# Performance work log

Measured on AMD Instinct MI355X. Metric: run time of the kernel, lower is better.

## Reference

```python
import jax, jax.numpy as jnp
import numpy as np

B, D, H, O, K = 8192, 256, 512, 64, 8


def setup_inputs() -> dict:
    key = jax.random.key(0)
    ks = jax.random.split(key, 4)
    s0 = 1.0 / np.sqrt(D)
    s1 = 1.0 / np.sqrt(H)
    return {
        "x": jax.random.normal(ks[0], (B, D), dtype=jnp.float32),
        "W0": jax.random.normal(ks[1], (K, D, H), dtype=jnp.float32) * s0,
        "b0": jnp.zeros((K, H), dtype=jnp.float32),
        "W1": jax.random.normal(ks[2], (K, H, H), dtype=jnp.float32) * s1,
        "b1": jnp.zeros((K, H), dtype=jnp.float32),
        "Wo": jax.random.normal(ks[3], (K, H, O), dtype=jnp.float32) * s1,
        "bo": jnp.zeros((K, O), dtype=jnp.float32),
    }


def reference(x, W0, b0, W1, b1, Wo, bo):
    # Hard one-hot router (non-differentiable int cast, as in the original)
    idx = jnp.mod(jnp.abs(x[:, 7] * 100.0).astype(jnp.int32), K)  # [B]
    att = jax.nn.one_hot(idx, K, dtype=x.dtype)  # [B, K]
    # Dense compute of ALL subpolicy MLPs (faithful to original wasteful scheme)
    h0 = jnp.tanh(jnp.einsum("bd,kdh->kbh", x, W0) + b0[:, None, :])   # [K,B,H]
    h1 = jnp.tanh(jnp.einsum("kbh,khg->kbg", h0, W1) + b1[:, None, :])  # [K,B,H]
    out = jnp.einsum("kbg,kgo->kbo", h1, Wo) + bo[:, None, :]           # [K,B,O]
    # mask with one-hot attention and sum over experts (tf.add_n of masked outputs)
    overall = jnp.einsum("kbo,bk->bo", out, att)                        # [B,O]
    return overall
```

## Files before the change

kernel.cpp:

```cpp
#include <hip/hip_runtime.h>

#define NB 8192
#define ND 256
#define NH 512
#define NO 64
#define NK 8
#define TB 32

typedef unsigned short u16;
using bf16x8 = __attribute__((ext_vector_type(8))) short;
using u16x8  = __attribute__((ext_vector_type(8))) unsigned short;
using f32x4  = __attribute__((ext_vector_type(4))) float;

__device__ __forceinline__ u16 bf16rne(float f) {
    unsigned u = __float_as_uint(f);
    return (u16)((u + 0x7FFFu + ((u >> 16) & 1u)) >> 16);
}

__device__ __forceinline__ float fast_tanh(float v) {
    float a = fabsf(v);
    float e = __expf(-2.0f * a);
    float t = (1.0f - e) * __builtin_amdgcn_rcpf(1.0f + e);
    return copysignf(t, v);
}


__global__ __launch_bounds__(256) void prep_kernel(
    const float* __restrict__ x,
    const float* __restrict__ W0, const float* __restrict__ W1, const float* __restrict__ Wo,
    int* __restrict__ wsI, u16* __restrict__ W0F, u16* __restrict__ W1F, u16* __restrict__ WoF) {
    const int bid = blockIdx.x, t = threadIdx.x;
    if (bid >= 832) {
        __shared__ int lc[NK], lbase[NK];
        if (t < NK) lc[t] = 0;
        __syncthreads();
        const int b = (bid - 832) * 256 + t;
        const float v = x[(size_t)b * ND + 7];
        const int e = ((int)fabsf(v * 100.0f)) & (NK - 1);
        const int slot = atomicAdd(&lc[e], 1);
        __syncthreads();
        if (t < NK) lbase[t] = atomicAdd(&wsI[t], lc[t]);
        __syncthreads();
        wsI[16 + e * NB + lbase[e] + slot] = b;
        return;
    }
    __shared__ u16 tile[64][76];
    const float* src; u16* dst; int C, NT, r0, c0;
    if (bid < 256) {
        int e = bid >> 5, tt = bid & 31; C = NH; NT = 32;
        src = W0 + (size_t)e * ND * NH; dst = W0F + (size_t)e * ND * NH;
        r0 = (tt >> 3) * 64; c0 = (tt & 7) * 64;
    } else if (bid < 768) {
        int i = bid - 256, e = i >> 6, tt = i & 63; C = NH; NT = 32;
        src = W1 + (size_t)e * NH * NH; dst = W1F + (size_t)e * NH * NH;
        r0 = (tt >> 3) * 64; c0 = (tt & 7) * 64;
    } else {
        int i = bid - 768, e = i >> 3, tt = i & 7; C = NO; NT = 4;
        src = Wo + (size_t)e * NH * NO; dst = WoF + (size_t)e * NH * NO;
        r0 = tt * 64; c0 = 0;
    }
    {
        const int r = t >> 2, cc = (t & 3) * 16;
        const float* p = src + (size_t)(r0 + r) * C + c0 + cc;
#pragma unroll
        for (int j = 0; j < 16; j += 4) {
            float4 v = *(const float4*)(p + j);
            ushort4 h;
            h.x = bf16rne(v.x); h.y = bf16rne(v.y); h.z = bf16rne(v.z); h.w = bf16rne(v.w);
            *(ushort4*)&tile[r][cc + j] = h;
        }
    }
    __syncthreads();
    {
#pragma unroll
        for (int i = 0; i < 2; ++i) {
            const int f = t + i * 256;
            const int lane = f & 63, s = f >> 6;
            const int ktl = s >> 2, ntl = s & 3;
            const int kt = (r0 >> 5) + ktl, nt = (c0 >> 4) + ntl;
            const int kloc = ktl * 32 + (lane >> 4) * 8, nloc = ntl * 16 + (lane & 15);
            u16x8 fr;
#pragma unroll
            for (int q = 0; q < 8; ++q) fr[q] = tile[kloc + q][nloc];
            *(u16x8*)(dst + (size_t)(((kt * NT + nt) << 6) + lane) * 8) = fr;
        }
    }
}

__global__ __launch_bounds__(512, 4) void mlp_kernel(
    const float* __restrict__ x,
    const float* __restrict__ b0, const float* __restrict__ b1, const float* __restrict__ bo,
    const int* __restrict__ wsI,
    const u16* __restrict__ W0F, const u16* __restrict__ W1F, const u16* __restrict__ WoF,
    float* __restrict__ out) {
    const int e = blockIdx.x & (NK - 1);
    const int tile = blockIdx.x >> 3;
    const int cnt = wsI[e];
    if (tile * TB >= cnt) return;

    __shared__ u16 L[32768];
    __shared__ int rows_s[TB];
    const int t = threadIdx.x;
    const int* bucket = wsI + 16 + e * NB;
    if (t < TB) {
        int lr = tile * TB + t;
        rows_s[t] = (lr < cnt) ? bucket[lr] : -1;
    }
    __syncthreads();

#pragma unroll
    for (int s = 0; s < 4; ++s) {
        int i = t + s * 512;
        int row = i >> 6, d4 = i & 63;
        int g = rows_s[row];
        float4 v = (g >= 0) ? *(const float4*)(x + (size_t)g * ND + d4 * 4)
                            : make_float4(0.f, 0.f, 0.f, 0.f);
        ushort4 h;
        h.x = bf16rne(v.x); h.y = bf16rne(v.y); h.z = bf16rne(v.z); h.w = bf16rne(v.w);
        int bb = (row * 512 + d4 * 8) ^ ((row & 7) << 4);
        *(ushort4*)&L[bb >> 1] = h;
    }
    __syncthreads();

    const int wid = t >> 6, l = t & 63;
    const int lrow = l & 15;
    const int lkb = (l >> 4) * 16;
    const int swz = (lrow & 7) << 4;

    f32x4 acc[2][4];
#pragma unroll
    for (int m = 0; m < 2; ++m)
#pragma unroll
        for (int j = 0; j < 4; ++j) acc[m][j] = (f32x4){0.f, 0.f, 0.f, 0.f};

    {
        const u16* P = W0F + (size_t)e * ND * NH + ((wid * 4) * 64 + l) * 8;
        bf16x8 cA[4], cB[4];
#pragma unroll
        for (int j = 0; j < 4; ++j) cA[j] = *(const bf16x8*)(P + j * 512);
#pragma unroll
        for (int kt = 0; kt < 8; kt += 2) {
#pragma unroll
            for (int j = 0; j < 4; ++j) cB[j] = *(const bf16x8*)(P + ((kt + 1) * 32 + j) * 512);
            {
                int kb = kt * 64;
                bf16x8 a0 = *(const bf16x8*)&L[((0 * 16 + lrow) * 512 + ((kb + lkb) ^ swz)) >> 1];
                bf16x8 a1 = *(const bf16x8*)&L[((1 * 16 + lrow) * 512 + ((kb + lkb) ^ swz)) >> 1];
#pragma unroll
                for (int j = 0; j < 4; ++j) {
                    acc[0][j] = __builtin_amdgcn_mfma_f32_16x16x32_bf16(a0, cA[j], acc[0][j], 0, 0, 0);
                    acc[1][j] = __builtin_amdgcn_mfma_f32_16x16x32_bf16(a1, cA[j], acc[1][j], 0, 0, 0);
                }
            }
            if (kt + 2 < 8) {
#pragma unroll
                for (int j = 0; j < 4; ++j) cA[j] = *(const bf16x8*)(P + ((kt + 2) * 32 + j) * 512);
            }
            {
                int kb = (kt + 1) * 64;
                bf16x8 a0 = *(const bf16x8*)&L[((0 * 16 + lrow) * 512 + ((kb + lkb) ^ swz)) >> 1];
                bf16x8 a1 = *(const bf16x8*)&L[((1 * 16 + lrow) * 512 + ((kb + lkb) ^ swz)) >> 1];
#pragma unroll
                for (int j = 0; j < 4; ++j) {
                    acc[0][j] = __builtin_amdgcn_mfma_f32_16x16x32_bf16(a0, cB[j], acc[0][j], 0, 0, 0);
                    acc[1][j] = __builtin_amdgcn_mfma_f32_16x16x32_bf16(a1, cB[j], acc[1][j], 0, 0, 0);
                }
            }
        }
#pragma unroll
        for (int m = 0; m < 2; ++m)
#pragma unroll
            for (int j = 0; j < 4; ++j) {
                int col = (wid * 4 + j) * 16 + lrow;
                float bias = b0[e * NH + col];
#pragma unroll
                for (int r = 0; r < 4; ++r) {
                    int row = m * 16 + (l >> 4) * 4 + r;
                    float tv = fast_tanh(acc[m][j][r] + bias);
                    int bb = 32768 + row * 1024 + ((col * 2) ^ ((row & 7) << 4));
                    L[bb >> 1] = bf16rne(tv);
                }
            }
    }
    __syncthreads();

    {
#pragma unroll
        for (int m = 0; m < 2; ++m)
#pragma unroll
            for (int j = 0; j < 4; ++j) acc[m][j] = (f32x4){0.f, 0.f, 0.f, 0.f};
        const u16* P = W1F + (size_t)e * NH * NH + ((wid * 4) * 64 + l) * 8;
        bf16x8 cA[4], cB[4];
#pragma unroll
        for (int j = 0; j < 4; ++j) cA[j] = *(const bf16x8*)(P + j * 512);
#pragma unroll
        for (int kt = 0; kt < 16; kt += 2) {
#pragma unroll
            for (int j = 0; j < 4; ++j) cB[j] = *(const bf16x8*)(P + ((kt + 1) * 32 + j) * 512);
            {
                int kb = 32768 + (kt * 64 + lkb);
                bf16x8 a0 = *(const bf16x8*)&L[((0 * 16 + lrow) * 1024 + 32768 + ((kt * 64 + lkb) ^ swz)) >> 1];
                bf16x8 a1 = *(const bf16x8*)&L[((1 * 16 + lrow) * 1024 + 32768 + ((kt * 64 + lkb) ^ swz)) >> 1];
                (void)kb;
#pragma unroll
                for (int j = 0; j < 4; ++j) {
                    acc[0][j] = __builtin_amdgcn_mfma_f32_16x16x32_bf16(a0, cA[j], acc[0][j], 0, 0, 0);
                    acc[1][j] = __builtin_amdgcn_mfma_f32_16x16x32_bf16(a1, cA[j], acc[1][j], 0, 0, 0);
                }
            }
            if (kt + 2 < 16) {
#pragma unroll
                for (int j = 0; j < 4; ++j) cA[j] = *(const bf16x8*)(P + ((kt + 2) * 32 + j) * 512);
            }
            {
                bf16x8 a0 = *(const bf16x8*)&L[((0 * 16 + lrow) * 1024 + 32768 + (((kt + 1) * 64 + lkb) ^ swz)) >> 1];
                bf16x8 a1 = *(const bf16x8*)&L[((1 * 16 + lrow) * 1024 + 32768 + (((kt + 1) * 64 + lkb) ^ swz)) >> 1];
#pragma unroll
                for (int j = 0; j < 4; ++j) {
                    acc[0][j] = __builtin_amdgcn_mfma_f32_16x16x32_bf16(a0, cB[j], acc[0][j], 0, 0, 0);
                    acc[1][j] = __builtin_amdgcn_mfma_f32_16x16x32_bf16(a1, cB[j], acc[1][j], 0, 0, 0);
                }
            }
        }
#pragma unroll
        for (int m = 0; m < 2; ++m)
#pragma unroll
            for (int j = 0; j < 4; ++j) {
                int col = (wid * 4 + j) * 16 + lrow;
                float bias = b1[e * NH + col];
#pragma unroll
                for (int r = 0; r < 4; ++r) {
                    int row = m * 16 + (l >> 4) * 4 + r;
                    float tv = fast_tanh(acc[m][j][r] + bias);
                    int bb = row * 1024 + ((col * 2) ^ ((row & 7) << 4));
                    L[bb >> 1] = bf16rne(tv);
                }
            }
    }
    __syncthreads();

    {
        const int nt = wid & 3, mt = wid >> 2;
        const u16* P = WoF + (size_t)e * NH * NO + (nt * 64 + l) * 8;
        f32x4 a2 = (f32x4){0.f, 0.f, 0.f, 0.f};
        bf16x8 wA = *(const bf16x8*)(P);
#pragma unroll
        for (int kt = 0; kt < 16; kt += 2) {
            bf16x8 wB = *(const bf16x8*)(P + ((kt + 1) * 4) * 512);
            {
                bf16x8 a = *(const bf16x8*)&L[((mt * 16 + lrow) * 1024 + ((kt * 64 + lkb) ^ swz)) >> 1];
                a2 = __builtin_amdgcn_mfma_f32_16x16x32_bf16(a, wA, a2, 0, 0, 0);
            }
            if (kt + 2 < 16) wA = *(const bf16x8*)(P + ((kt + 2) * 4) * 512);
            {
                bf16x8 a = *(const bf16x8*)&L[((mt * 16 + lrow) * 1024 + (((kt + 1) * 64 + lkb) ^ swz)) >> 1];
                a2 = __builtin_amdgcn_mfma_f32_16x16x32_bf16(a, wB, a2, 0, 0, 0);
            }
        }
        int col = nt * 16 + lrow;
        float bias = bo[e * NO + col];
#pragma unroll
        for (int r = 0; r < 4; ++r) {
            int row = mt * 16 + (l >> 4) * 4 + r;
            int g = rows_s[row];
            if (g >= 0) out[(size_t)g * NO + col] = a2[r] + bias;
        }
    }
}

extern "C" void kernel_launch(void* const* d_in, const int* in_sizes, int n_in,
                              void* d_out, int out_size, void* d_ws, size_t ws_size,
                              hipStream_t stream) {
    const float* x  = (const float*)d_in[0];
    const float* W0 = (const float*)d_in[1];
    const float* b0 = (const float*)d_in[2];
    const float* W1 = (const float*)d_in[3];
    const float* b1 = (const float*)d_in[4];
    const float* Wo = (const float*)d_in[5];
    const float* bo = (const float*)d_in[6];
    float* out = (float*)d_out;
    int* wsI = (int*)d_ws;
    u16* W0F = (u16*)((char*)d_ws + (512 << 10));
    u16* W1F = W0F + (size_t)NK * ND * NH;
    u16* WoF = W1F + (size_t)NK * NH * NH;

    hipMemsetAsync(wsI, 0, 64, stream);
    prep_kernel<<<864, 256, 0, stream>>>(x, W0, W1, Wo, wsI, W0F, W1F, WoF);
    mlp_kernel<<<NK * (NB / TB), 512, 0, stream>>>(x, b0, b1, bo, wsI, W0F, W1F, WoF, out);
}
```

Before: 103.2 us.

## Deepen MFMA operand prefetch to 3 stages and restructure weight prep into K-slab blocks

The three GEMM loops in the MLP kernel switch from a 2-deep double buffer to a 4-slot ring that prefetches both weight fragments and LDS activation fragments three k-steps ahead, with s_setprio raised around MFMA bursts. The launch bound drops from 4 to 2 blocks per SIMD to leave registers for the deeper buffers. The prep kernel now converts one contiguous 32-row K-slab per block with fewer, larger blocks, which simplifies the layout transform. The cost is higher register pressure and lower occupancy in exchange for hiding memory latency.

```diff
diff --git a/kernel.cpp b/kernel.cpp
--- a/kernel.cpp
+++ b/kernel.cpp
@@ -30,11 +30,11 @@
     const float* __restrict__ W0, const float* __restrict__ W1, const float* __restrict__ Wo,
     int* __restrict__ wsI, u16* __restrict__ W0F, u16* __restrict__ W1F, u16* __restrict__ WoF) {
     const int bid = blockIdx.x, t = threadIdx.x;
-    if (bid >= 832) {
+    if (bid >= 320) {
         __shared__ int lc[NK], lbase[NK];
         if (t < NK) lc[t] = 0;
         __syncthreads();
-        const int b = (bid - 832) * 256 + t;
+        const int b = (bid - 320) * 256 + t;
         const float v = x[(size_t)b * ND + 7];
         const int e = ((int)fabsf(v * 100.0f)) & (NK - 1);
         const int slot = atomicAdd(&lc[e], 1);
@@ -44,50 +44,41 @@
         wsI[16 + e * NB + lbase[e] + slot] = b;
         return;
     }
-    __shared__ u16 tile[64][76];
-    const float* src; u16* dst; int C, NT, r0, c0;
-    if (bid < 256) {
-        int e = bid >> 5, tt = bid & 31; C = NH; NT = 32;
-        src = W0 + (size_t)e * ND * NH; dst = W0F + (size_t)e * ND * NH;
-        r0 = (tt >> 3) * 64; c0 = (tt & 7) * 64;
-    } else if (bid < 768) {
-        int i = bid - 256, e = i >> 6, tt = i & 63; C = NH; NT = 32;
-        src = W1 + (size_t)e * NH * NH; dst = W1F + (size_t)e * NH * NH;
-        r0 = (tt >> 3) * 64; c0 = (tt & 7) * 64;
+    __shared__ u16 slab[32 * 524];
+    const float* src; u16* dst; int C, NT, sh;
+    if (bid < 64) {
+        int e = bid >> 3, kt = bid & 7; C = NH; NT = 32; sh = 7;
+        src = W0 + ((size_t)e * ND + kt * 32) * NH;
+        dst = W0F + (size_t)(e * 8 + kt) * 32 * 512;
+    } else if (bid < 192) {
+        int i = bid - 64, e = i >> 4, kt = i & 15; C = NH; NT = 32; sh = 7;
+        src = W1 + ((size_t)e * NH + kt * 32) * NH;
+        dst = W1F + (size_t)(e * 16 + kt) * 32 * 512;
     } else {
-        int i = bid - 768, e = i >> 3, tt = i & 7; C = NO; NT = 4;
-        src = Wo + (size_t)e * NH * NO; dst = WoF + (size_t)e * NH * NO;
-        r0 = tt * 64; c0 = 0;
-    }
-    {
-        const int r = t >> 2, cc = (t & 3) * 16;
-        const float* p = src + (size_t)(r0 + r) * C + c0 + cc;
-#pragma unroll
-        for (int j = 0; j < 16; j += 4) {
-            float4 v = *(const float4*)(p + j);
-            ushort4 h;
-            h.x = bf16rne(v.x); h.y = bf16rne(v.y); h.z = bf16rne(v.z); h.w = bf16rne(v.w);
-            *(ushort4*)&tile[r][cc + j] = h;
-        }
-    }
-    __syncthreads();
-    {
-#pragma unroll
-        for (int i = 0; i < 2; ++i) {
-            const int f = t + i * 256;
-            const int lane = f & 63, s = f >> 6;
-            const int ktl = s >> 2, ntl = s & 3;
-            const int kt = (r0 >> 5) + ktl, nt = (c0 >> 4) + ntl;
-            const int kloc = ktl * 32 + (lane >> 4) * 8, nloc = ntl * 16 + (lane & 15);
-            u16x8 fr;
-#pragma unroll
-            for (int q = 0; q < 8; ++q) fr[q] = tile[kloc + q][nloc];
-            *(u16x8*)(dst + (size_t)(((kt * NT + nt) << 6) + lane) * 8) = fr;
-        }
-    }
-}
-
-__global__ __launch_bounds__(512, 4) void mlp_kernel(
+        int i = bid - 192, e = i >> 4, kt = i & 15; C = NO; NT = 4; sh = 4;
+        src = Wo + ((size_t)e * NH + kt * 32) * NO;
+        dst = WoF + (size_t)(e * 16 + kt) * 4 * 512;
+    }
+    const int c4 = C >> 2, total4 = 8 * C;
+    for (int f = t; f < total4; f += 256) {
+        float4 v = *(const float4*)(src + ((size_t)f << 2));
+        ushort4 h;
+        h.x = bf16rne(v.x); h.y = bf16rne(v.y); h.z = bf16rne(v.z); h.w = bf16rne(v.w);
+        int row = f >> sh, col4 = f & (c4 - 1);
+        *(ushort4*)&slab[row * 524 + col4 * 4] = h;
+    }
+    __syncthreads();
+    for (int f = t; f < NT * 64; f += 256) {
+        const int lane = f & 63, nt = f >> 6;
+        const int kloc = (lane >> 4) << 3, nc = nt * 16 + (lane & 15);
+        u16x8 fr;
+#pragma unroll
+        for (int q = 0; q < 8; ++q) fr[q] = slab[(kloc + q) * 524 + nc];
+        *(u16x8*)(dst + (size_t)f * 8) = fr;
+    }
+}
+
+__global__ __launch_bounds__(512, 2) void mlp_kernel(
     const float* __restrict__ x,
     const float* __restrict__ b0, const float* __restrict__ b1, const float* __restrict__ bo,
     const int* __restrict__ wsI,
@@ -134,38 +125,34 @@
         for (int j = 0; j < 4; ++j) acc[m][j] = (f32x4){0.f, 0.f, 0.f, 0.f};
 
     {
-        const u16* P = W0F + (size_t)e * ND * NH + ((wid * 4) * 64 + l) * 8;
-        bf16x8 cA[4], cB[4];
-#pragma unroll
-        for (int j = 0; j < 4; ++j) cA[j] = *(const bf16x8*)(P + j * 512);
-#pragma unroll
-        for (int kt = 0; kt < 8; kt += 2) {
-#pragma unroll
-            for (int j = 0; j < 4; ++j) cB[j] = *(const bf16x8*)(P + ((kt + 1) * 32 + j) * 512);
-            {
-                int kb = kt * 64;
-                bf16x8 a0 = *(const bf16x8*)&L[((0 * 16 + lrow) * 512 + ((kb + lkb) ^ swz)) >> 1];
-                bf16x8 a1 = *(const bf16x8*)&L[((1 * 16 + lrow) * 512 + ((kb + lkb) ^ swz)) >> 1];
-#pragma unroll
-                for (int j = 0; j < 4; ++j) {
-                    acc[0][j] = __builtin_amdgcn_mfma_f32_16x16x32_bf16(a0, cA[j], acc[0][j], 0, 0, 0);
-                    acc[1][j] = __builtin_amdgcn_mfma_f32_16x16x32_bf16(a1, cA[j], acc[1][j], 0, 0, 0);
-                }
-            }
-            if (kt + 2 < 8) {
-#pragma unroll
-                for (int j = 0; j < 4; ++j) cA[j] = *(const bf16x8*)(P + ((kt + 2) * 32 + j) * 512);
-            }
-            {
-                int kb = (kt + 1) * 64;
-                bf16x8 a0 = *(const bf16x8*)&L[((0 * 16 + lrow) * 512 + ((kb + lkb) ^ swz)) >> 1];
-                bf16x8 a1 = *(const bf16x8*)&L[((1 * 16 + lrow) * 512 + ((kb + lkb) ^ swz)) >> 1];
-#pragma unroll
-                for (int j = 0; j < 4; ++j) {
-                    acc[0][j] = __builtin_amdgcn_mfma_f32_16x16x32_bf16(a0, cB[j], acc[0][j], 0, 0, 0);
-                    acc[1][j] = __builtin_amdgcn_mfma_f32_16x16x32_bf16(a1, cB[j], acc[1][j], 0, 0, 0);
-                }
-            }
+        const u16* P = W0F + (size_t)e * (8 * 32 * 512) + (wid * 4) * 512 + l * 8;
+        bf16x8 bb[4][4], aa[4][2];
+#pragma unroll
+        for (int s = 0; s < 3; ++s) {
+#pragma unroll
+            for (int j = 0; j < 4; ++j) bb[s][j] = *(const bf16x8*)(P + (s * 32 + j) * 512);
+#pragma unroll
+            for (int m = 0; m < 2; ++m)
+                aa[s][m] = *(const bf16x8*)&L[((m * 16 + lrow) * 512 + ((s * 64 + lkb) ^ swz)) >> 1];
+        }
+#pragma unroll
+        for (int kt = 0; kt < 8; ++kt) {
+            if (kt + 3 < 8) {
+                const int p = (kt + 3) & 3;
+#pragma unroll
+                for (int j = 0; j < 4; ++j) bb[p][j] = *(const bf16x8*)(P + ((kt + 3) * 32 + j) * 512);
+#pragma unroll
+                for (int m = 0; m < 2; ++m)
+                    aa[p][m] = *(const bf16x8*)&L[((m * 16 + lrow) * 512 + (((kt + 3) * 64 + lkb) ^ swz)) >> 1];
+            }
+            const int c = kt & 3;
+            __builtin_amdgcn_s_setprio(1);
+#pragma unroll
+            for (int j = 0; j < 4; ++j) {
+                acc[0][j] = __builtin_amdgcn_mfma_f32_16x16x32_bf16(aa[c][0], bb[c][j], acc[0][j], 0, 0, 0);
+                acc[1][j] = __builtin_amdgcn_mfma_f32_16x16x32_bf16(aa[c][1], bb[c][j], acc[1][j], 0, 0, 0);
+            }
+            __builtin_amdgcn_s_setprio(0);
         }
 #pragma unroll
         for (int m = 0; m < 2; ++m)
@@ -177,8 +164,8 @@
                 for (int r = 0; r < 4; ++r) {
                     int row = m * 16 + (l >> 4) * 4 + r;
                     float tv = fast_tanh(acc[m][j][r] + bias);
-                    int bb = 32768 + row * 1024 + ((col * 2) ^ ((row & 7) << 4));
-                    L[bb >> 1] = bf16rne(tv);
+                    int bb2 = 32768 + row * 1024 + ((col * 2) ^ ((row & 7) << 4));
+                    L[bb2 >> 1] = bf16rne(tv);
                 }
             }
     }
@@ -189,38 +176,34 @@
         for (int m = 0; m < 2; ++m)
 #pragma unroll
             for (int j = 0; j < 4; ++j) acc[m][j] = (f32x4){0.f, 0.f, 0.f, 0.f};
-        const u16* P = W1F + (size_t)e * NH * NH + ((wid * 4) * 64 + l) * 8;
-        bf16x8 cA[4], cB[4];
-#pragma unroll
-        for (int j = 0; j < 4; ++j) cA[j] = *(const bf16x8*)(P + j * 512);
-#pragma unroll
-        for (int kt = 0; kt < 16; kt += 2) {
-#pragma unroll
-            for (int j = 0; j < 4; ++j) cB[j] = *(const bf16x8*)(P + ((kt + 1) * 32 + j) * 512);
-            {
-                int kb = 32768 + (kt * 64 + lkb);
-                bf16x8 a0 = *(const bf16x8*)&L[((0 * 16 + lrow) * 1024 + 32768 + ((kt * 64 + lkb) ^ swz)) >> 1];
-                bf16x8 a1 = *(const bf16x8*)&L[((1 * 16 + lrow) * 1024 + 32768 + ((kt * 64 + lkb) ^ swz)) >> 1];
-                (void)kb;
-#pragma unroll
-                for (int j = 0; j < 4; ++j) {
-                    acc[0][j] = __builtin_amdgcn_mfma_f32_16x16x32_bf16(a0, cA[j], acc[0][j], 0, 0, 0);
-                    acc[1][j] = __builtin_amdgcn_mfma_f32_16x16x32_bf16(a1, cA[j], acc[1][j], 0, 0, 0);
-                }
-            }
-            if (kt + 2 < 16) {
-#pragma unroll
-                for (int j = 0; j < 4; ++j) cA[j] = *(const bf16x8*)(P + ((kt + 2) * 32 + j) * 512);
-            }
-            {
-                bf16x8 a0 = *(const bf16x8*)&L[((0 * 16 + lrow) * 1024 + 32768 + (((kt + 1) * 64 + lkb) ^ swz)) >> 1];
-                bf16x8 a1 = *(const bf16x8*)&L[((1 * 16 + lrow) * 1024 + 32768 + (((kt + 1) * 64 + lkb) ^ swz)) >> 1];
-#pragma unroll
-                for (int j = 0; j < 4; ++j) {
-                    acc[0][j] = __builtin_amdgcn_mfma_f32_16x16x32_bf16(a0, cB[j], acc[0][j], 0, 0, 0);
-                    acc[1][j] = __builtin_amdgcn_mfma_f32_16x16x32_bf16(a1, cB[j], acc[1][j], 0, 0, 0);
-                }
-            }
+        const u16* P = W1F + (size_t)e * (16 * 32 * 512) + (wid * 4) * 512 + l * 8;
+        bf16x8 bb[4][4], aa[4][2];
+#pragma unroll
+        for (int s = 0; s < 3; ++s) {
+#pragma unroll
+            for (int j = 0; j < 4; ++j) bb[s][j] = *(const bf16x8*)(P + (s * 32 + j) * 512);
+#pragma unroll
+            for (int m = 0; m < 2; ++m)
+                aa[s][m] = *(const bf16x8*)&L[((m * 16 + lrow) * 1024 + 32768 + ((s * 64 + lkb) ^ swz)) >> 1];
+        }
+#pragma unroll
+        for (int kt = 0; kt < 16; ++kt) {
+            if (kt + 3 < 16) {
+                const int p = (kt + 3) & 3;
+#pragma unroll
+                for (int j = 0; j < 4; ++j) bb[p][j] = *(const bf16x8*)(P + ((kt + 3) * 32 + j) * 512);
+#pragma unroll
+                for (int m = 0; m < 2; ++m)
+                    aa[p][m] = *(const bf16x8*)&L[((m * 16 + lrow) * 1024 + 32768 + (((kt + 3) * 64 + lkb) ^ swz)) >> 1];
+            }
+            const int c = kt & 3;
+            __builtin_amdgcn_s_setprio(1);
+#pragma unroll
+            for (int j = 0; j < 4; ++j) {
+                acc[0][j] = __builtin_amdgcn_mfma_f32_16x16x32_bf16(aa[c][0], bb[c][j], acc[0][j], 0, 0, 0);
+                acc[1][j] = __builtin_amdgcn_mfma_f32_16x16x32_bf16(aa[c][1], bb[c][j], acc[1][j], 0, 0, 0);
+            }
+            __builtin_amdgcn_s_setprio(0);
         }
 #pragma unroll
         for (int m = 0; m < 2; ++m)
@@ -232,8 +215,8 @@
                 for (int r = 0; r < 4; ++r) {
                     int row = m * 16 + (l >> 4) * 4 + r;
                     float tv = fast_tanh(acc[m][j][r] + bias);
-                    int bb = row * 1024 + ((col * 2) ^ ((row & 7) << 4));
-                    L[bb >> 1] = bf16rne(tv);
+                    int bb2 = row * 1024 + ((col * 2) ^ ((row & 7) << 4));
+                    L[bb2 >> 1] = bf16rne(tv);
                 }
             }
     }
@@ -241,21 +224,23 @@
 
     {
         const int nt = wid & 3, mt = wid >> 2;
-        const u16* P = WoF + (size_t)e * NH * NO + (nt * 64 + l) * 8;
+        const u16* P = WoF + (size_t)e * (16 * 4 * 512) + nt * 512 + l * 8;
         f32x4 a2 = (f32x4){0.f, 0.f, 0.f, 0.f};
-        bf16x8 wA = *(const bf16x8*)(P);
-#pragma unroll
-        for (int kt = 0; kt < 16; kt += 2) {
-            bf16x8 wB = *(const bf16x8*)(P + ((kt + 1) * 4) * 512);
-            {
-                bf16x8 a = *(const bf16x8*)&L[((mt * 16 + lrow) * 1024 + ((kt * 64 + lkb) ^ swz)) >> 1];
-                a2 = __builtin_amdgcn_mfma_f32_16x16x32_bf16(a, wA, a2, 0, 0, 0);
-            }
-            if (kt + 2 < 16) wA = *(const bf16x8*)(P + ((kt + 2) * 4) * 512);
-            {
-                bf16x8 a = *(const bf16x8*)&L[((mt * 16 + lrow) * 1024 + (((kt + 1) * 64 + lkb) ^ swz)) >> 1];
-                a2 = __builtin_amdgcn_mfma_f32_16x16x32_bf16(a, wB, a2, 0, 0, 0);
-            }
+        bf16x8 wb[4], wa[4];
+#pragma unroll
+        for (int s = 0; s < 3; ++s) {
+            wb[s] = *(const bf16x8*)(P + (s * 4) * 512);
+            wa[s] = *(const bf16x8*)&L[((mt * 16 + lrow) * 1024 + ((s * 64 + lkb) ^ swz)) >> 1];
+        }
+#pragma unroll
+        for (int kt = 0; kt < 16; ++kt) {
+            if (kt + 3 < 16) {
+                const int p = (kt + 3) & 3;
+                wb[p] = *(const bf16x8*)(P + ((kt + 3) * 4) * 512);
+                wa[p] = *(const bf16x8*)&L[((mt * 16 + lrow) * 1024 + (((kt + 3) * 64 + lkb) ^ swz)) >> 1];
+            }
+            const int c = kt & 3;
+            a2 = __builtin_amdgcn_mfma_f32_16x16x32_bf16(wa[c], wb[c], a2, 0, 0, 0);
         }
         int col = nt * 16 + lrow;
         float bias = bo[e * NO + col];
@@ -285,6 +270,6 @@
     u16* WoF = W1F + (size_t)NK * NH * NH;
 
     hipMemsetAsync(wsI, 0, 64, stream);
-    prep_kernel<<<864, 256, 0, stream>>>(x, W0, W1, Wo, wsI, W0F, W1F, WoF);
+    prep_kernel<<<352, 256, 0, stream>>>(x, W0, W1, Wo, wsI, W0F, W1F, WoF);
     mlp_kernel<<<NK * (NB / TB), 512, 0, stream>>>(x, b0, b1, bo, wsI, W0F, W1F, WoF, out);
 }
```

Result: slower. 111.1 us (+7.7%).
